# Optimization experiments

Hardware: AMD Instinct MI355X
Metric: run time of the kernel (lower is better)

The kernel has to match this reference:

```python
import jax, jax.numpy as jnp
import numpy as np

N_NODES = 50000
N_EDGES = 400000
H, D = 4, 32  # num_heads, per-head dim
NEG_SLOPE = 0.1


def setup_inputs() -> dict:
    key = jax.random.key(0)
    ks = jax.random.split(key, 12)
    inp = {
        'features': jax.random.normal(ks[0], (N_NODES, 256), jnp.float32) * 0.1,
        'src': jax.random.randint(ks[1], (N_EDGES,), 0, N_NODES, jnp.int32),
        'dst': jax.random.randint(ks[2], (N_EDGES,), 0, N_NODES, jnp.int32),
        'w': jax.random.uniform(ks[3], (N_EDGES,), jnp.float32),
        'W1': jax.random.normal(ks[4], (256, 128), jnp.float32) * 0.05,
        'al1': jax.random.normal(ks[5], (H, D), jnp.float32) * 0.1,
        'ar1': jax.random.normal(ks[6], (H, D), jnp.float32) * 0.1,
        'W2': jax.random.normal(ks[7], (128, 128), jnp.float32) * 0.05,
        'al2': jax.random.normal(ks[8], (H, D), jnp.float32) * 0.1,
        'ar2': jax.random.normal(ks[9], (H, D), jnp.float32) * 0.1,
        'Wout': jax.random.normal(ks[10], (256, 128), jnp.float32) * 0.05,
        'bout': jnp.zeros((128,), jnp.float32),
    }
    return inp


def _gat_layer(x, W, al, ar, src, dst, w):
    # x: [N, in_dim] -> ft: [N, H, D]
    ft = (x @ W).reshape(-1, H, D)
    el = jnp.einsum('nhd,hd->nh', ft, al)  # left attention logits per node
    er = jnp.einsum('nhd,hd->nh', ft, ar)
    # edge logits: leaky_relu(el[src] + er[dst]), then edge-weight scaling
    e = jax.nn.leaky_relu(el[src] + er[dst], negative_slope=NEG_SLOPE)  # [E, H]
    e = w[:, None] * e
    # segment softmax over incoming edges of each destination node
    m = jax.ops.segment_max(e, dst, num_segments=N_NODES)  # [N, H]
    a = jnp.exp(e - m[dst])
    s = jax.ops.segment_sum(a, dst, num_segments=N_NODES)
    a = a / s[dst]  # [E, H]
    # weighted scatter-sum aggregation: rst[dst] += a * ft[src]
    msg = ft[src] * a[:, :, None]  # [E, H, D]
    rst = jax.ops.segment_sum(msg, dst, num_segments=N_NODES)  # [N, H, D]
    # activation=relu, then concat heads (contiguous -> reshape)
    return jax.nn.relu(rst).reshape(-1, H * D)


def reference(features, src, dst, w, W1, al1, ar1, W2, al2, ar2, Wout, bout):
    x1 = _gat_layer(features, W1, al1, ar1, src, dst, w)  # [N, 128]
    x2 = _gat_layer(x1, W2, al2, ar2, src, dst, w)        # [N, 128]
    h = jnp.concatenate([x1, x2], axis=-1)                # [N, 256]
    return h @ Wout + bout                                # [N, 128]
```

## Files before the change

kernel.cpp:

```cpp
#include <hip/hip_runtime.h>
#include <math.h>

#define NHEAD 4
#define HDIM 32
#define NEG_SLOPE 0.1f

typedef unsigned short u16;
typedef unsigned int u32;
typedef _Float16 f16;
typedef f16 f16x2 __attribute__((ext_vector_type(2)));
typedef f16 f16x4 __attribute__((ext_vector_type(4)));
typedef f16 f16x8 __attribute__((ext_vector_type(8)));
typedef float f32x4 __attribute__((ext_vector_type(4)));

#define GLLDS16(g, l) __builtin_amdgcn_global_load_lds( \
    (const __attribute__((address_space(1))) void*)(g), \
    (__attribute__((address_space(3))) void*)(l), 16, 0, 0)


__device__ __forceinline__ void cast_panel(const float* __restrict__ W,
                                           const float* __restrict__ al,
                                           const float* __restrict__ ar,
                                           u16* __restrict__ bp, int t, int NC) {
    int per_kt = NC * 16;
    int kt = t / per_kt;
    int rem = t - kt * per_kt;
    int nt = rem >> 8;
    int w32 = rem & 255;
    int kg = w32 >> 6;
    int col = (w32 >> 2) & 15;
    int kp = (w32 & 3) * 2;
    int n = nt * 16 + col;
    int k = kt * 32 + kg * 8 + kp;
    float v0 = 0.f, v1 = 0.f;
    if (n < 128) {
        v0 = W[(size_t)k * 128 + n];
        v1 = W[(size_t)(k + 1) * 128 + n];
    } else if (n < 136) {
        const float* av = (n < 132) ? al : ar;
        int h = (n < 132) ? (n - 128) : (n - 132);
        float s0 = 0.f, s1 = 0.f;
        for (int d = 0; d < 32; d++) {
            float a = av[h * 32 + d];
            s0 += W[(size_t)k * 128 + h * 32 + d] * a;
            s1 += W[(size_t)(k + 1) * 128 + h * 32 + d] * a;
        }
        v0 = s0; v1 = s1;
    }
    f16x2 p;
    p.x = (f16)v0; p.y = (f16)v1;
    *(f16x2*)&((u32*)bp)[t] = p;
}

__global__ void histcast_k(const int* __restrict__ dst, int* __restrict__ cnt, int E,
                           const float* __restrict__ W1, const float* __restrict__ al1,
                           const float* __restrict__ ar1, u16* __restrict__ b1,
                           const float* __restrict__ W2, const float* __restrict__ al2,
                           const float* __restrict__ ar2, u16* __restrict__ b2,
                           const float* __restrict__ W3, u16* __restrict__ b3) {
    int t = blockIdx.x * 256 + threadIdx.x;
    if (t < E) atomicAdd(&cnt[dst[t]], 1);
    if (t < 18432) cast_panel(W1, al1, ar1, b1, t, 144);
    else if (t < 27648) cast_panel(W2, al2, ar2, b2, t - 18432, 144);
    else if (t < 44032) cast_panel(W3, nullptr, nullptr, b3, t - 27648, 128);
}


__global__ void assign_k(const int* __restrict__ cnt, int* __restrict__ start,
                         int* __restrict__ ctr, int N) {
    __shared__ int s[256];
    __shared__ int base;
    int t = threadIdx.x;
    int i = blockIdx.x * 256 + t;
    int v = (i < N) ? cnt[i] : 0;
    s[t] = v;
    __syncthreads();
    int incl = v;
    for (int off = 1; off < 256; off <<= 1) {
        int add = (t >= off) ? s[t - off] : 0;
        __syncthreads();
        incl += add;
        s[t] = incl;
        __syncthreads();
    }
    if (t == 255) base = atomicAdd(ctr, incl);
    __syncthreads();
    if (i < N) start[i] = base + incl - v;
}

__global__ void scatter_k(const int* __restrict__ src, const int* __restrict__ dst,
                          const float* __restrict__ w, const int* __restrict__ start,
                          int* __restrict__ fill, int2* __restrict__ edge_s, int E) {
    int e = blockIdx.x * 256 + threadIdx.x;
    if (e >= E) return;
    int d = dst[e];
    int p = atomicAdd(&fill[d], 1);
    edge_s[start[d] + p] = make_int2(src[e], __float_as_int(w[e]));
}


template <int NT>
__global__ __launch_bounds__(256) void gemm_h_k(
        const void* __restrict__ Av, int a_is_f16, int lda,
        const u16* __restrict__ Bp,
        const float* __restrict__ bias, float* __restrict__ Cf,
        u16* __restrict__ Ch, float* __restrict__ el, float* __restrict__ er,
        int M, int K) {
    __shared__ u16 As[2048];
    __shared__ u16 Bs[NT * 512];
    int tid = threadIdx.x;
    int w = tid >> 6, lane = tid & 63;
    int row0 = blockIdx.x * 64;
    int mrow = lane & 15;

    f32x4 acc[NT];
#pragma unroll
    for (int nt = 0; nt < NT; nt++) acc[nt] = (f32x4){0.f, 0.f, 0.f, 0.f};

    for (int k0 = 0; k0 < K; k0 += 32) {
        int kt = k0 >> 5;
#pragma unroll
        for (int i = 0; i < (NT * 64 + 255) / 256; i++) {
            int c = tid + i * 256;
            if (c < NT * 64)
                GLLDS16(Bp + (size_t)kt * (NT * 512) + (size_t)c * 8, &Bs[c * 8]);
        }
        if (a_is_f16) {
            const u16* Ah = (const u16*)Av;
            int c = tid;
            int rblk = c >> 6, kg = (c >> 4) & 3, rr = c & 15;
            GLLDS16(Ah + (size_t)(row0 + rblk * 16 + rr) * lda + k0 + kg * 8,
                    &As[c * 8]);
        } else {
            const float* Af = (const float*)Av;
            int c = tid;
            int rblk = c >> 6, kg = (c >> 4) & 3, rr = c & 15;
            int row = min(row0 + rblk * 16 + rr, M - 1);
            const float* ap = &Af[(size_t)row * lda + k0 + kg * 8];
            float4 v0 = *(const float4*)ap;
            float4 v1 = *(const float4*)(ap + 4);
            f16x8 p;
            p[0] = (f16)v0.x; p[1] = (f16)v0.y; p[2] = (f16)v0.z; p[3] = (f16)v0.w;
            p[4] = (f16)v1.x; p[5] = (f16)v1.y; p[6] = (f16)v1.z; p[7] = (f16)v1.w;
            *(f16x8*)&As[c * 8] = p;
        }
        __syncthreads();

        f16x8 ah = *(const f16x8*)&As[w * 512 + lane * 8];
#pragma unroll
        for (int nt = 0; nt < NT; nt++) {
            f16x8 bh = *(const f16x8*)&Bs[nt * 512 + lane * 8];
            acc[nt] = __builtin_amdgcn_mfma_f32_16x16x32_f16(ah, bh, acc[nt], 0, 0, 0);
        }
        __syncthreads();
    }

    int rbase = row0 + w * 16 + (lane >> 4) * 4;
#pragma unroll
    for (int nt = 0; nt < 8; nt++) {
        int col = nt * 16 + mrow;
        float bv = bias ? bias[col] : 0.f;
        f32x4 v = acc[nt];
#pragma unroll
        for (int reg = 0; reg < 4; reg++) {
            int rr = rbase + reg;
            if (rr < M) {
                float val = v[reg] + bv;
                if (Cf) Cf[(size_t)rr * 128 + col] = val;
                if (Ch) *(f16*)&Ch[(size_t)rr * 128 + col] = (f16)val;
            }
        }
    }
    if (NT == 9) {
        f32x4 v = acc[8];
#pragma unroll
        for (int reg = 0; reg < 4; reg++) {
            int rr = rbase + reg;
            if (rr < M) {
                if (mrow < 4) el[rr * 4 + mrow] = v[reg];
                else if (mrow < 8) er[rr * 4 + (mrow - 4)] = v[reg];
            }
        }
    }
}


__device__ __forceinline__ float lrelu(float x) {
    return x > 0.f ? x : NEG_SLOPE * x;
}

__global__ __launch_bounds__(256) void agg_k(const u32* __restrict__ fth2,
                                             const float4* __restrict__ el4,
                                             const float4* __restrict__ er4,
                                             const int2* __restrict__ edge_s,
                                             const int* __restrict__ start,
                                             const int* __restrict__ cnt,
                                             u16* __restrict__ xcat,
                                             int ooff, int N, int ngroups) {
    __shared__ float4 sA[256];
    __shared__ int sS[256];
    int wv = threadIdx.x >> 6;
    int lane = threadIdx.x & 63;
    int head = lane >> 4;
    for (int g = blockIdx.x; g < ngroups; g += gridDim.x) {
        int n = g * 4 + wv;
        if (n >= N) continue;
        int r0 = start[n], deg = cnt[n];
        u16* op = &xcat[(size_t)n * 256 + ooff + 2 * lane];
        if (deg == 0) {
            *(u32*)op = 0;
            continue;
        }
        float4 ern = er4[n];
        float acc0 = 0.f, acc1 = 0.f;
        if (deg <= 64) {
            float4 a = make_float4(0.f, 0.f, 0.f, 0.f);
            int s = 0;
            if (lane < deg) {
                int2 ep = edge_s[r0 + lane];
                s = ep.x;
                float we = __int_as_float(ep.y);
                float4 e = el4[s];
                a.x = __expf(we * lrelu(e.x + ern.x));
                a.y = __expf(we * lrelu(e.y + ern.y));
                a.z = __expf(we * lrelu(e.z + ern.z));
                a.w = __expf(we * lrelu(e.w + ern.w));
            }
            float4 sm = a;
            for (int m = 1; m < deg; m <<= 1) {
                sm.x += __shfl_xor(sm.x, m);
                sm.y += __shfl_xor(sm.y, m);
                sm.z += __shfl_xor(sm.z, m);
                sm.w += __shfl_xor(sm.w, m);
            }
            a.x *= __builtin_amdgcn_rcpf(sm.x);
            a.y *= __builtin_amdgcn_rcpf(sm.y);
            a.z *= __builtin_amdgcn_rcpf(sm.z);
            a.w *= __builtin_amdgcn_rcpf(sm.w);
            sA[wv * 64 + lane] = a;
            sS[wv * 64 + lane] = s;
            const float* sAf = (const float*)&sA[wv * 64];
            const int* sSp = &sS[wv * 64];
            int i = 0;
            for (; i + 8 <= deg; i += 8) {
                float wg[8];
                u32 pp[8];
#pragma unroll
                for (int j = 0; j < 8; j++) {
                    wg[j] = sAf[(i + j) * 4 + head];
                    pp[j] = fth2[(size_t)sSp[i + j] * 64 + lane];
                }
#pragma unroll
                for (int j = 0; j < 8; j++) {
                    f16x2 hp = *(const f16x2*)&pp[j];
                    acc0 += wg[j] * (float)hp.x;
                    acc1 += wg[j] * (float)hp.y;
                }
            }
            for (; i < deg; i++) {
                float wgt = sAf[i * 4 + head];
                u32 p = fth2[(size_t)sSp[i] * 64 + lane];
                f16x2 hp = *(const f16x2*)&p;
                acc0 += wgt * (float)hp.x;
                acc1 += wgt * (float)hp.y;
            }
        } else {
            float4 mx = make_float4(-INFINITY, -INFINITY, -INFINITY, -INFINITY);
            for (int i = lane; i < deg; i += 64) {
                int2 ep = edge_s[r0 + i];
                float we = __int_as_float(ep.y);
                float4 e = el4[ep.x];
                mx.x = fmaxf(mx.x, we * lrelu(e.x + ern.x));
                mx.y = fmaxf(mx.y, we * lrelu(e.y + ern.y));
                mx.z = fmaxf(mx.z, we * lrelu(e.z + ern.z));
                mx.w = fmaxf(mx.w, we * lrelu(e.w + ern.w));
            }
            for (int m = 32; m >= 1; m >>= 1) {
                mx.x = fmaxf(mx.x, __shfl_xor(mx.x, m));
                mx.y = fmaxf(mx.y, __shfl_xor(mx.y, m));
                mx.z = fmaxf(mx.z, __shfl_xor(mx.z, m));
                mx.w = fmaxf(mx.w, __shfl_xor(mx.w, m));
            }
            float4 sm = make_float4(0.f, 0.f, 0.f, 0.f);
            for (int i = lane; i < deg; i += 64) {
                int2 ep = edge_s[r0 + i];
                float we = __int_as_float(ep.y);
                float4 e = el4[ep.x];
                sm.x += __expf(we * lrelu(e.x + ern.x) - mx.x);
                sm.y += __expf(we * lrelu(e.y + ern.y) - mx.y);
                sm.z += __expf(we * lrelu(e.z + ern.z) - mx.z);
                sm.w += __expf(we * lrelu(e.w + ern.w) - mx.w);
            }
            for (int m = 32; m >= 1; m >>= 1) {
                sm.x += __shfl_xor(sm.x, m);
                sm.y += __shfl_xor(sm.y, m);
                sm.z += __shfl_xor(sm.z, m);
                sm.w += __shfl_xor(sm.w, m);
            }
            float4 inv;
            inv.x = 1.f / sm.x; inv.y = 1.f / sm.y;
            inv.z = 1.f / sm.z; inv.w = 1.f / sm.w;
            for (int i = 0; i < deg; i++) {
                int2 ep = edge_s[r0 + i];
                int si = ep.x;
                float we = __int_as_float(ep.y);
                float4 e = el4[si];
                float ax = __expf(we * lrelu(e.x + ern.x) - mx.x) * inv.x;
                float ay = __expf(we * lrelu(e.y + ern.y) - mx.y) * inv.y;
                float az = __expf(we * lrelu(e.z + ern.z) - mx.z) * inv.z;
                float aw = __expf(we * lrelu(e.w + ern.w) - mx.w) * inv.w;
                float wgt = head == 0 ? ax : (head == 1 ? ay : (head == 2 ? az : aw));
                u32 p = fth2[(size_t)si * 64 + lane];
                f16x2 hp = *(const f16x2*)&p;
                acc0 += wgt * (float)hp.x;
                acc1 += wgt * (float)hp.y;
            }
        }
        f16x2 hv;
        hv.x = (f16)fmaxf(acc0, 0.f);
        hv.y = (f16)fmaxf(acc1, 0.f);
        *(f16x2*)op = hv;
    }
}


extern "C" void kernel_launch(void* const* d_in, const int* in_sizes, int n_in,
                              void* d_out, int out_size, void* d_ws, size_t ws_size,
                              hipStream_t stream) {
    const float* features = (const float*)d_in[0];
    const int* src = (const int*)d_in[1];
    const int* dst = (const int*)d_in[2];
    const float* w = (const float*)d_in[3];
    const float* W1 = (const float*)d_in[4];
    const float* al1 = (const float*)d_in[5];
    const float* ar1 = (const float*)d_in[6];
    const float* W2 = (const float*)d_in[7];
    const float* al2 = (const float*)d_in[8];
    const float* ar2 = (const float*)d_in[9];
    const float* Wout = (const float*)d_in[10];
    const float* bout = (const float*)d_in[11];
    float* out = (float*)d_out;

    int N = in_sizes[0] / 256;
    int E = in_sizes[1];
    int Mpad = ((N + 127) / 128) * 128;

    char* ws = (char*)d_ws;
    size_t off = 0;
    auto alloc = [&](size_t bytes) -> void* {
        void* p = ws + off;
        off = (off + bytes + 255) & ~(size_t)255;
        return p;
    };
    size_t Nr = ((size_t)N * 4 + 255) & ~(size_t)255;
    int* cnt = (int*)alloc(2 * Nr + 256);
    int* fill = (int*)((char*)cnt + Nr);
    int* ctr = (int*)((char*)cnt + 2 * Nr);
    int* start = (int*)alloc((size_t)N * 4);
    int2* edge_s = (int2*)alloc((size_t)E * 8);
    u16* fth = (u16*)alloc((size_t)Mpad * 128 * 2);
    float* el = (float*)alloc((size_t)N * 4 * 4);
    float* er = (float*)alloc((size_t)N * 4 * 4);
    u16* xcat = (u16*)alloc((size_t)Mpad * 256 * 2);
    u16* b1 = (u16*)alloc((size_t)18432 * 4);
    u16* b2 = (u16*)alloc((size_t)9216 * 4);
    u16* b3 = (u16*)alloc((size_t)16384 * 4);
    (void)ws_size; (void)n_in; (void)out_size;

    hipMemsetAsync(cnt, 0, 2 * Nr + 256, stream);

    int eb = (E + 255) / 256;
    int nb = (N + 255) / 256;
    int ng = (N + 3) / 4;
    int ab = ng < 2048 ? ng : 2048;
    int gb = Mpad / 64;

    histcast_k<<<eb, 256, 0, stream>>>(dst, cnt, E, W1, al1, ar1, b1,
                                       W2, al2, ar2, b2, Wout, b3);
    assign_k<<<nb, 256, 0, stream>>>(cnt, start, ctr, N);
    scatter_k<<<eb, 256, 0, stream>>>(src, dst, w, start, fill, edge_s, E);

    gemm_h_k<9><<<gb, 256, 0, stream>>>(features, 0, 256, b1, nullptr,
                                        nullptr, fth, el, er, N, 256);
    agg_k<<<ab, 256, 0, stream>>>((const u32*)fth, (const float4*)el, (const float4*)er,
                                  edge_s, start, cnt, xcat, 0, N, ng);

    gemm_h_k<9><<<gb, 256, 0, stream>>>(xcat, 1, 256, b2, nullptr,
                                        nullptr, fth, el, er, N, 128);
    agg_k<<<ab, 256, 0, stream>>>((const u32*)fth, (const float4*)el, (const float4*)er,
                                  edge_s, start, cnt, xcat, 128, N, ng);

    gemm_h_k<8><<<gb, 256, 0, stream>>>(xcat, 1, 256, b3, bout,
                                        out, nullptr, nullptr, nullptr, N, 256);
}
```

Baseline: 258.7 us.

## Fuse all GAT stages into one persistent kernel with grid-wide barriers

Replaces eight separate kernel launches with a single persistent kernel whose blocks loop over work in each phase and meet at a hand-rolled atomic grid barrier. The grid is sized from occupancy, capped at 1024 blocks. Layer-1 GEMM is placed after scatter without a barrier, so it overlaps the edge sort. The goal is to remove launch gaps and tail idle time between small phases. The costs are barrier spin overhead, reduced parallelism in the grid-strided GEMM and agg loops, and reliance on all blocks being co-resident.

```diff
diff --git a/kernel.cpp b/kernel.cpp
--- a/kernel.cpp
+++ b/kernel.cpp
@@ -1,21 +1,46 @@
 #include <hip/hip_runtime.h>
 #include <math.h>
 
-#define NHEAD 4
-#define HDIM 32
 #define NEG_SLOPE 0.1f
 
 typedef unsigned short u16;
 typedef unsigned int u32;
 typedef _Float16 f16;
 typedef f16 f16x2 __attribute__((ext_vector_type(2)));
-typedef f16 f16x4 __attribute__((ext_vector_type(4)));
 typedef f16 f16x8 __attribute__((ext_vector_type(8)));
 typedef float f32x4 __attribute__((ext_vector_type(4)));
 
 #define GLLDS16(g, l) __builtin_amdgcn_global_load_lds( \
     (const __attribute__((address_space(1))) void*)(g), \
     (__attribute__((address_space(3))) void*)(l), 16, 0, 0)
+
+struct P {
+    const float* features; const int* src; const int* dst; const float* w;
+    const float* W1; const float* al1; const float* ar1;
+    const float* W2; const float* al2; const float* ar2;
+    const float* W3; const float* bout; float* out;
+    int* cnt; int* fill; int* ctr; int* bar; int* start; int2* edge_s;
+    u16* fth; float* el; float* er; u16* xcat;
+    u16* b1; u16* b2; u16* b3;
+    int N, E, Mpad;
+};
+
+
+__device__ __forceinline__ void gsync(int* bar, int slot) {
+    __syncthreads();
+    if (threadIdx.x == 0) {
+        __threadfence();
+        int* a = &bar[slot * 16];
+        int prev = __hip_atomic_fetch_add(a, 1, __ATOMIC_ACQ_REL, __HIP_MEMORY_SCOPE_AGENT);
+        if (prev == (int)gridDim.x - 1) {
+            __hip_atomic_store(a + 1, 1, __ATOMIC_RELEASE, __HIP_MEMORY_SCOPE_AGENT);
+        } else {
+            while (!__hip_atomic_load(a + 1, __ATOMIC_ACQUIRE, __HIP_MEMORY_SCOPE_AGENT))
+                __builtin_amdgcn_s_sleep(4);
+        }
+    }
+    __syncthreads();
+}
 
 
 __device__ __forceinline__ void cast_panel(const float* __restrict__ W,
@@ -38,175 +63,177 @@
         v1 = W[(size_t)(k + 1) * 128 + n];
     } else if (n < 136) {
         const float* av = (n < 132) ? al : ar;
-        int h = (n < 132) ? (n - 128) : (n - 132);
-        float s0 = 0.f, s1 = 0.f;
-        for (int d = 0; d < 32; d++) {
-            float a = av[h * 32 + d];
-            s0 += W[(size_t)k * 128 + h * 32 + d] * a;
-            s1 += W[(size_t)(k + 1) * 128 + h * 32 + d] * a;
-        }
-        v0 = s0; v1 = s1;
-    }
-    f16x2 p;
-    p.x = (f16)v0; p.y = (f16)v1;
-    *(f16x2*)&((u32*)bp)[t] = p;
-}
-
-__global__ void histcast_k(const int* __restrict__ dst, int* __restrict__ cnt, int E,
-                           const float* __restrict__ W1, const float* __restrict__ al1,
-                           const float* __restrict__ ar1, u16* __restrict__ b1,
-                           const float* __restrict__ W2, const float* __restrict__ al2,
-                           const float* __restrict__ ar2, u16* __restrict__ b2,
-                           const float* __restrict__ W3, u16* __restrict__ b3) {
-    int t = blockIdx.x * 256 + threadIdx.x;
-    if (t < E) atomicAdd(&cnt[dst[t]], 1);
-    if (t < 18432) cast_panel(W1, al1, ar1, b1, t, 144);
-    else if (t < 27648) cast_panel(W2, al2, ar2, b2, t - 18432, 144);
-    else if (t < 44032) cast_panel(W3, nullptr, nullptr, b3, t - 27648, 128);
-}
-
-
-__global__ void assign_k(const int* __restrict__ cnt, int* __restrict__ start,
-                         int* __restrict__ ctr, int N) {
-    __shared__ int s[256];
-    __shared__ int base;
+        if (av) {
+            int h = (n < 132) ? (n - 128) : (n - 132);
+            float s0 = 0.f, s1 = 0.f;
+            for (int d = 0; d < 32; d++) {
+                float a = av[h * 32 + d];
+                s0 += W[(size_t)k * 128 + h * 32 + d] * a;
+                s1 += W[(size_t)(k + 1) * 128 + h * 32 + d] * a;
+            }
+            v0 = s0; v1 = s1;
+        }
+    }
+    f16x2 pk;
+    pk.x = (f16)v0; pk.y = (f16)v1;
+    *(f16x2*)&((u32*)bp)[t] = pk;
+}
+
+
+__device__ void phase_hist(const P& p) {
+    int gsz = gridDim.x * 256;
+    for (int t = blockIdx.x * 256 + threadIdx.x; t < p.E; t += gsz) {
+        atomicAdd(&p.cnt[p.dst[t]], 1);
+        if (t < 18432) cast_panel(p.W1, p.al1, p.ar1, p.b1, t, 144);
+        else if (t < 27648) cast_panel(p.W2, p.al2, p.ar2, p.b2, t - 18432, 144);
+        else if (t < 46080) cast_panel(p.W3, nullptr, nullptr, p.b3, t - 27648, 144);
+    }
+}
+
+__device__ void phase_assign(const P& p, char* sh) {
+    int* s = (int*)sh;
+    int* basep = s + 256;
     int t = threadIdx.x;
-    int i = blockIdx.x * 256 + t;
-    int v = (i < N) ? cnt[i] : 0;
-    s[t] = v;
-    __syncthreads();
-    int incl = v;
-    for (int off = 1; off < 256; off <<= 1) {
-        int add = (t >= off) ? s[t - off] : 0;
+    int chunks = (p.N + 255) >> 8;
+    for (int c = blockIdx.x; c < chunks; c += gridDim.x) {
+        int i = c * 256 + t;
+        int v = (i < p.N) ? p.cnt[i] : 0;
+        s[t] = v;
         __syncthreads();
-        incl += add;
-        s[t] = incl;
+        int incl = v;
+        for (int off = 1; off < 256; off <<= 1) {
+            int add = (t >= off) ? s[t - off] : 0;
+            __syncthreads();
+            incl += add;
+            s[t] = incl;
+            __syncthreads();
+        }
+        if (t == 255) *basep = atomicAdd(p.ctr, incl);
         __syncthreads();
-    }
-    if (t == 255) base = atomicAdd(ctr, incl);
-    __syncthreads();
-    if (i < N) start[i] = base + incl - v;
-}
-
-__global__ void scatter_k(const int* __restrict__ src, const int* __restrict__ dst,
-                          const float* __restrict__ w, const int* __restrict__ start,
-                          int* __restrict__ fill, int2* __restrict__ edge_s, int E) {
-    int e = blockIdx.x * 256 + threadIdx.x;
-    if (e >= E) return;
-    int d = dst[e];
-    int p = atomicAdd(&fill[d], 1);
-    edge_s[start[d] + p] = make_int2(src[e], __float_as_int(w[e]));
-}
-
-
-template <int NT>
-__global__ __launch_bounds__(256) void gemm_h_k(
-        const void* __restrict__ Av, int a_is_f16, int lda,
-        const u16* __restrict__ Bp,
-        const float* __restrict__ bias, float* __restrict__ Cf,
-        u16* __restrict__ Ch, float* __restrict__ el, float* __restrict__ er,
-        int M, int K) {
-    __shared__ u16 As[2048];
-    __shared__ u16 Bs[NT * 512];
+        if (i < p.N) p.start[i] = *basep + incl - v;
+        __syncthreads();
+    }
+}
+
+__device__ void phase_scatter(const P& p) {
+    int gsz = gridDim.x * 256;
+    for (int e = blockIdx.x * 256 + threadIdx.x; e < p.E; e += gsz) {
+        int d = p.dst[e];
+        int pos = atomicAdd(&p.fill[d], 1);
+        p.edge_s[p.start[d] + pos] = make_int2(p.src[e], __float_as_int(p.w[e]));
+    }
+}
+
+__device__ void gemm_core(const void* Av, int a_is_f16, int lda, const u16* Bp,
+                          const float* bias, float* Cf, u16* Ch,
+                          float* el, float* er, int M, int K, char* shmem) {
+    u16* As = (u16*)shmem;
+    u16* Bs = (u16*)(shmem + 4096);
     int tid = threadIdx.x;
-    int w = tid >> 6, lane = tid & 63;
-    int row0 = blockIdx.x * 64;
+    int wv = tid >> 6, lane = tid & 63;
     int mrow = lane & 15;
-
-    f32x4 acc[NT];
-#pragma unroll
-    for (int nt = 0; nt < NT; nt++) acc[nt] = (f32x4){0.f, 0.f, 0.f, 0.f};
-
-    for (int k0 = 0; k0 < K; k0 += 32) {
-        int kt = k0 >> 5;
-#pragma unroll
-        for (int i = 0; i < (NT * 64 + 255) / 256; i++) {
-            int c = tid + i * 256;
-            if (c < NT * 64)
-                GLLDS16(Bp + (size_t)kt * (NT * 512) + (size_t)c * 8, &Bs[c * 8]);
-        }
-        if (a_is_f16) {
-            const u16* Ah = (const u16*)Av;
+    int tiles = (M + 63) >> 6;
+    for (int t = blockIdx.x; t < tiles; t += gridDim.x) {
+        int row0 = t * 64;
+        f32x4 acc[9];
+#pragma unroll
+        for (int nt = 0; nt < 9; nt++) acc[nt] = (f32x4){0.f, 0.f, 0.f, 0.f};
+        for (int k0 = 0; k0 < K; k0 += 32) {
+            int kt = k0 >> 5;
+#pragma unroll
+            for (int i = 0; i < 3; i++) {
+                int c = tid + i * 256;
+                if (c < 576)
+                    GLLDS16(Bp + (size_t)kt * 4608 + (size_t)c * 8, &Bs[c * 8]);
+            }
             int c = tid;
             int rblk = c >> 6, kg = (c >> 4) & 3, rr = c & 15;
-            GLLDS16(Ah + (size_t)(row0 + rblk * 16 + rr) * lda + k0 + kg * 8,
-                    &As[c * 8]);
-        } else {
-            const float* Af = (const float*)Av;
-            int c = tid;
-            int rblk = c >> 6, kg = (c >> 4) & 3, rr = c & 15;
-            int row = min(row0 + rblk * 16 + rr, M - 1);
-            const float* ap = &Af[(size_t)row * lda + k0 + kg * 8];
-            float4 v0 = *(const float4*)ap;
-            float4 v1 = *(const float4*)(ap + 4);
-            f16x8 p;
-            p[0] = (f16)v0.x; p[1] = (f16)v0.y; p[2] = (f16)v0.z; p[3] = (f16)v0.w;
-            p[4] = (f16)v1.x; p[5] = (f16)v1.y; p[6] = (f16)v1.z; p[7] = (f16)v1.w;
-            *(f16x8*)&As[c * 8] = p;
-        }
-        __syncthreads();
-
-        f16x8 ah = *(const f16x8*)&As[w * 512 + lane * 8];
-#pragma unroll
-        for (int nt = 0; nt < NT; nt++) {
-            f16x8 bh = *(const f16x8*)&Bs[nt * 512 + lane * 8];
-            acc[nt] = __builtin_amdgcn_mfma_f32_16x16x32_f16(ah, bh, acc[nt], 0, 0, 0);
-        }
-        __syncthreads();
-    }
-
-    int rbase = row0 + w * 16 + (lane >> 4) * 4;
-#pragma unroll
-    for (int nt = 0; nt < 8; nt++) {
-        int col = nt * 16 + mrow;
-        float bv = bias ? bias[col] : 0.f;
-        f32x4 v = acc[nt];
-#pragma unroll
-        for (int reg = 0; reg < 4; reg++) {
-            int rr = rbase + reg;
-            if (rr < M) {
-                float val = v[reg] + bv;
-                if (Cf) Cf[(size_t)rr * 128 + col] = val;
-                if (Ch) *(f16*)&Ch[(size_t)rr * 128 + col] = (f16)val;
-            }
-        }
-    }
-    if (NT == 9) {
-        f32x4 v = acc[8];
-#pragma unroll
-        for (int reg = 0; reg < 4; reg++) {
-            int rr = rbase + reg;
-            if (rr < M) {
-                if (mrow < 4) el[rr * 4 + mrow] = v[reg];
-                else if (mrow < 8) er[rr * 4 + (mrow - 4)] = v[reg];
-            }
-        }
-    }
-}
-
+            if (a_is_f16) {
+                const u16* Ah = (const u16*)Av;
+                GLLDS16(Ah + (size_t)(row0 + rblk * 16 + rr) * lda + k0 + kg * 8,
+                        &As[c * 8]);
+            } else {
+                const float* Af = (const float*)Av;
+                int row = row0 + rblk * 16 + rr;
+                if (row > M - 1) row = M - 1;
+                const float* ap = &Af[(size_t)row * lda + k0 + kg * 8];
+                float4 v0 = *(const float4*)ap;
+                float4 v1 = *(const float4*)(ap + 4);
+                f16x8 pk;
+                pk[0] = (f16)v0.x; pk[1] = (f16)v0.y; pk[2] = (f16)v0.z; pk[3] = (f16)v0.w;
+                pk[4] = (f16)v1.x; pk[5] = (f16)v1.y; pk[6] = (f16)v1.z; pk[7] = (f16)v1.w;
+                *(f16x8*)&As[c * 8] = pk;
+            }
+            __syncthreads();
+            f16x8 ah = *(const f16x8*)&As[wv * 512 + lane * 8];
+#pragma unroll
+            for (int nt = 0; nt < 9; nt++) {
+                f16x8 bh = *(const f16x8*)&Bs[nt * 512 + lane * 8];
+                acc[nt] = __builtin_amdgcn_mfma_f32_16x16x32_f16(ah, bh, acc[nt], 0, 0, 0);
+            }
+            __syncthreads();
+        }
+        int rbase = row0 + wv * 16 + (lane >> 4) * 4;
+#pragma unroll
+        for (int nt = 0; nt < 8; nt++) {
+            int col = nt * 16 + mrow;
+            float bv = bias ? bias[col] : 0.f;
+            f32x4 v = acc[nt];
+#pragma unroll
+            for (int reg = 0; reg < 4; reg++) {
+                int r2 = rbase + reg;
+                if (r2 < M) {
+                    float val = v[reg] + bv;
+                    if (Cf) Cf[(size_t)r2 * 128 + col] = val;
+                    if (Ch) *(f16*)&Ch[(size_t)r2 * 128 + col] = (f16)val;
+                }
+            }
+        }
+        if (el) {
+            f32x4 v = acc[8];
+#pragma unroll
+            for (int reg = 0; reg < 4; reg++) {
+                int r2 = rbase + reg;
+                if (r2 < M) {
+                    if (mrow < 4) el[r2 * 4 + mrow] = v[reg];
+                    else if (mrow < 8) er[r2 * 4 + (mrow - 4)] = v[reg];
+                }
+            }
+        }
+    }
+}
+
+__device__ void gemm_sel(const P& p, int which, char* sh) {
+    if (which == 1)
+        gemm_core(p.features, 0, 256, p.b1, nullptr, nullptr, p.fth, p.el, p.er,
+                  p.N, 256, sh);
+    else if (which == 2)
+        gemm_core(p.xcat, 1, 256, p.b2, nullptr, nullptr, p.fth, p.el, p.er,
+                  p.N, 128, sh);
+    else
+        gemm_core(p.xcat, 1, 256, p.b3, p.bout, p.out, nullptr, nullptr, nullptr,
+                  p.N, 256, sh);
+}
 
 __device__ __forceinline__ float lrelu(float x) {
     return x > 0.f ? x : NEG_SLOPE * x;
 }
 
-__global__ __launch_bounds__(256) void agg_k(const u32* __restrict__ fth2,
-                                             const float4* __restrict__ el4,
-                                             const float4* __restrict__ er4,
-                                             const int2* __restrict__ edge_s,
-                                             const int* __restrict__ start,
-                                             const int* __restrict__ cnt,
-                                             u16* __restrict__ xcat,
-                                             int ooff, int N, int ngroups) {
-    __shared__ float4 sA[256];
-    __shared__ int sS[256];
+__device__ void phase_agg(const P& p, int ooff, char* sh) {
+    float4* sA = (float4*)sh;
+    int* sS = (int*)(sh + 4096);
+    const u32* fth2 = (const u32*)p.fth;
+    const float4* el4 = (const float4*)p.el;
+    const float4* er4 = (const float4*)p.er;
     int wv = threadIdx.x >> 6;
     int lane = threadIdx.x & 63;
     int head = lane >> 4;
+    int ngroups = (p.N + 3) >> 2;
     for (int g = blockIdx.x; g < ngroups; g += gridDim.x) {
         int n = g * 4 + wv;
-        if (n >= N) continue;
-        int r0 = start[n], deg = cnt[n];
-        u16* op = &xcat[(size_t)n * 256 + ooff + 2 * lane];
+        if (n >= p.N) continue;
+        int r0 = p.start[n], deg = p.cnt[n];
+        u16* op = &p.xcat[(size_t)n * 256 + ooff + 2 * lane];
         if (deg == 0) {
             *(u32*)op = 0;
             continue;
@@ -217,7 +244,7 @@
             float4 a = make_float4(0.f, 0.f, 0.f, 0.f);
             int s = 0;
             if (lane < deg) {
-                int2 ep = edge_s[r0 + lane];
+                int2 ep = p.edge_s[r0 + lane];
                 s = ep.x;
                 float we = __int_as_float(ep.y);
                 float4 e = el4[s];
@@ -259,15 +286,15 @@
             }
             for (; i < deg; i++) {
                 float wgt = sAf[i * 4 + head];
-                u32 p = fth2[(size_t)sSp[i] * 64 + lane];
-                f16x2 hp = *(const f16x2*)&p;
+                u32 pv = fth2[(size_t)sSp[i] * 64 + lane];
+                f16x2 hp = *(const f16x2*)&pv;
                 acc0 += wgt * (float)hp.x;
                 acc1 += wgt * (float)hp.y;
             }
         } else {
             float4 mx = make_float4(-INFINITY, -INFINITY, -INFINITY, -INFINITY);
             for (int i = lane; i < deg; i += 64) {
-                int2 ep = edge_s[r0 + i];
+                int2 ep = p.edge_s[r0 + i];
                 float we = __int_as_float(ep.y);
                 float4 e = el4[ep.x];
                 mx.x = fmaxf(mx.x, we * lrelu(e.x + ern.x));
@@ -283,7 +310,7 @@
             }
             float4 sm = make_float4(0.f, 0.f, 0.f, 0.f);
             for (int i = lane; i < deg; i += 64) {
-                int2 ep = edge_s[r0 + i];
+                int2 ep = p.edge_s[r0 + i];
                 float we = __int_as_float(ep.y);
                 float4 e = el4[ep.x];
                 sm.x += __expf(we * lrelu(e.x + ern.x) - mx.x);
@@ -301,7 +328,7 @@
             inv.x = 1.f / sm.x; inv.y = 1.f / sm.y;
             inv.z = 1.f / sm.z; inv.w = 1.f / sm.w;
             for (int i = 0; i < deg; i++) {
-                int2 ep = edge_s[r0 + i];
+                int2 ep = p.edge_s[r0 + i];
                 int si = ep.x;
                 float we = __int_as_float(ep.y);
                 float4 e = el4[si];
@@ -310,8 +337,8 @@
                 float az = __expf(we * lrelu(e.z + ern.z) - mx.z) * inv.z;
                 float aw = __expf(we * lrelu(e.w + ern.w) - mx.w) * inv.w;
                 float wgt = head == 0 ? ax : (head == 1 ? ay : (head == 2 ? az : aw));
-                u32 p = fth2[(size_t)si * 64 + lane];
-                f16x2 hp = *(const f16x2*)&p;
+                u32 pv = fth2[(size_t)si * 64 + lane];
+                f16x2 hp = *(const f16x2*)&pv;
                 acc0 += wgt * (float)hp.x;
                 acc1 += wgt * (float)hp.y;
             }
@@ -324,72 +351,108 @@
 }
 
 
+__global__ __launch_bounds__(256, 4) void k_fused(P p) {
+    alignas(16) __shared__ char sh[13312];
+    phase_hist(p);
+    gsync(p.bar, 0);
+    phase_assign(p, sh);
+    gsync(p.bar, 1);
+    phase_scatter(p);
+    gemm_sel(p, 1, sh);
+    gsync(p.bar, 2);
+    phase_agg(p, 0, sh);
+    gsync(p.bar, 3);
+    gemm_sel(p, 2, sh);
+    gsync(p.bar, 4);
+    phase_agg(p, 128, sh);
+    gsync(p.bar, 5);
+    gemm_sel(p, 3, sh);
+}
+
+
+__global__ __launch_bounds__(256) void k_p1(P p) { phase_hist(p); }
+__global__ __launch_bounds__(256) void k_assign(P p) {
+    alignas(16) __shared__ char sh[2048];
+    phase_assign(p, sh);
+}
+__global__ __launch_bounds__(256) void k_scatter(P p) { phase_scatter(p); }
+__global__ __launch_bounds__(256) void k_gemm(P p, int which) {
+    alignas(16) __shared__ char sh[13312];
+    gemm_sel(p, which, sh);
+}
+__global__ __launch_bounds__(256) void k_agg(P p, int ooff) {
+    alignas(16) __shared__ char sh[8192];
+    phase_agg(p, ooff, sh);
+}
+
+
 extern "C" void kernel_launch(void* const* d_in, const int* in_sizes, int n_in,
                               void* d_out, int out_size, void* d_ws, size_t ws_size,
                               hipStream_t stream) {
-    const float* features = (const float*)d_in[0];
-    const int* src = (const int*)d_in[1];
-    const int* dst = (const int*)d_in[2];
-    const float* w = (const float*)d_in[3];
-    const float* W1 = (const float*)d_in[4];
-    const float* al1 = (const float*)d_in[5];
-    const float* ar1 = (const float*)d_in[6];
-    const float* W2 = (const float*)d_in[7];
-    const float* al2 = (const float*)d_in[8];
-    const float* ar2 = (const float*)d_in[9];
-    const float* Wout = (const float*)d_in[10];
-    const float* bout = (const float*)d_in[11];
-    float* out = (float*)d_out;
-
-    int N = in_sizes[0] / 256;
-    int E = in_sizes[1];
-    int Mpad = ((N + 127) / 128) * 128;
+    P p;
+    p.features = (const float*)d_in[0];
+    p.src = (const int*)d_in[1];
+    p.dst = (const int*)d_in[2];
+    p.w = (const float*)d_in[3];
+    p.W1 = (const float*)d_in[4];
+    p.al1 = (const float*)d_in[5];
+    p.ar1 = (const float*)d_in[6];
+    p.W2 = (const float*)d_in[7];
+    p.al2 = (const float*)d_in[8];
+    p.ar2 = (const float*)d_in[9];
+    p.W3 = (const float*)d_in[10];
+    p.bout = (const float*)d_in[11];
+    p.out = (float*)d_out;
+
+    p.N = in_sizes[0] / 256;
+    p.E = in_sizes[1];
+    p.Mpad = ((p.N + 127) / 128) * 128;
 
     char* ws = (char*)d_ws;
     size_t off = 0;
     auto alloc = [&](size_t bytes) -> void* {
-        void* p = ws + off;
+        void* q = ws + off;
         off = (off + bytes + 255) & ~(size_t)255;
-        return p;
+        return q;
     };
-    size_t Nr = ((size_t)N * 4 + 255) & ~(size_t)255;
-    int* cnt = (int*)alloc(2 * Nr + 256);
-    int* fill = (int*)((char*)cnt + Nr);
-    int* ctr = (int*)((char*)cnt + 2 * Nr);
-    int* start = (int*)alloc((size_t)N * 4);
-    int2* edge_s = (int2*)alloc((size_t)E * 8);
-    u16* fth = (u16*)alloc((size_t)Mpad * 128 * 2);
-    float* el = (float*)alloc((size_t)N * 4 * 4);
-    float* er = (float*)alloc((size_t)N * 4 * 4);
-    u16* xcat = (u16*)alloc((size_t)Mpad * 256 * 2);
-    u16* b1 = (u16*)alloc((size_t)18432 * 4);
-    u16* b2 = (u16*)alloc((size_t)9216 * 4);
-    u16* b3 = (u16*)alloc((size_t)16384 * 4);
+    size_t Nr = ((size_t)p.N * 4 + 255) & ~(size_t)255;
+    p.cnt = (int*)alloc(2 * Nr + 1024);
+    p.fill = (int*)((char*)p.cnt + Nr);
+    p.ctr = (int*)((char*)p.cnt + 2 * Nr);
+    p.bar = p.ctr + 64;
+    p.start = (int*)alloc((size_t)p.N * 4);
+    p.edge_s = (int2*)alloc((size_t)p.E * 8);
+    p.fth = (u16*)alloc((size_t)p.Mpad * 128 * 2);
+    p.el = (float*)alloc((size_t)p.N * 4 * 4);
+    p.er = (float*)alloc((size_t)p.N * 4 * 4);
+    p.xcat = (u16*)alloc((size_t)p.Mpad * 256 * 2);
+    p.b1 = (u16*)alloc((size_t)18432 * 4);
+    p.b2 = (u16*)alloc((size_t)9216 * 4);
+    p.b3 = (u16*)alloc((size_t)18432 * 4);
     (void)ws_size; (void)n_in; (void)out_size;
 
-    hipMemsetAsync(cnt, 0, 2 * Nr + 256, stream);
-
-    int eb = (E + 255) / 256;
-    int nb = (N + 255) / 256;
-    int ng = (N + 3) / 4;
-    int ab = ng < 2048 ? ng : 2048;
-    int gb = Mpad / 64;
-
-    histcast_k<<<eb, 256, 0, stream>>>(dst, cnt, E, W1, al1, ar1, b1,
-                                       W2, al2, ar2, b2, Wout, b3);
-    assign_k<<<nb, 256, 0, stream>>>(cnt, start, ctr, N);
-    scatter_k<<<eb, 256, 0, stream>>>(src, dst, w, start, fill, edge_s, E);
-
-    gemm_h_k<9><<<gb, 256, 0, stream>>>(features, 0, 256, b1, nullptr,
-                                        nullptr, fth, el, er, N, 256);
-    agg_k<<<ab, 256, 0, stream>>>((const u32*)fth, (const float4*)el, (const float4*)er,
-                                  edge_s, start, cnt, xcat, 0, N, ng);
-
-    gemm_h_k<9><<<gb, 256, 0, stream>>>(xcat, 1, 256, b2, nullptr,
-                                        nullptr, fth, el, er, N, 128);
-    agg_k<<<ab, 256, 0, stream>>>((const u32*)fth, (const float4*)el, (const float4*)er,
-                                  edge_s, start, cnt, xcat, 128, N, ng);
-
-    gemm_h_k<8><<<gb, 256, 0, stream>>>(xcat, 1, 256, b3, bout,
-                                        out, nullptr, nullptr, nullptr, N, 256);
-}
+    hipMemsetAsync(p.cnt, 0, 2 * Nr + 1024, stream);
+
+    static int s_grid = -2;
+    if (s_grid == -2) {
+        int b = 0;
+        hipError_t e = hipOccupancyMaxActiveBlocksPerMultiprocessor(&b, k_fused, 256, 0);
+        s_grid = (e == hipSuccess && b >= 1) ? (b * 256 < 1024 ? b * 256 : 1024) : 0;
+    }
+
+    if (s_grid > 0) {
+        k_fused<<<s_grid, 256, 0, stream>>>(p);
+    } else {
+        int eb = (p.E + 255) / 256;
+        int cb = (p.N + 255) / 256;
+        int gb = p.Mpad / 64;
+        k_p1<<<eb, 256, 0, stream>>>(p);
+        k_assign<<<cb, 256, 0, stream>>>(p);
+        k_scatter<<<eb, 256, 0, stream>>>(p);
+        k_gemm<<<gb, 256, 0, stream>>>(p, 1);
+        k_agg<<<2048, 256, 0, stream>>>(p, 0);
+        k_gemm<<<gb, 256, 0, stream>>>(p, 2);
+        k_agg<<<2048, 256, 0, stream>>>(p, 128);
+        k_gemm<<<gb, 256, 0, stream>>>(p, 3);
+    }
+}
```

Measured after the change: 795.8 us. 208% more time.

## Merge edge scatter into first GEMM launch and double GEMM K-step

Applied to the files above, without the earlier changes.

The edge-scatter kernel becomes extra blocks of the first projection GEMM launch, so CSR construction and the layer-1 GEMM run side by side in one launch instead of back to back. The GEMM body moves into a shared device function that now stages 64 K-columns per iteration (two 32-wide slices), which halves the barrier count and gives more MFMA work per sync. In exchange each block uses more shared memory, which may lower occupancy, and the grid of the merged launch now holds two unrelated block types.

```diff
diff --git a/kernel.cpp b/kernel.cpp
--- a/kernel.cpp
+++ b/kernel.cpp
@@ -1,15 +1,12 @@
 #include <hip/hip_runtime.h>
 #include <math.h>
 
-#define NHEAD 4
-#define HDIM 32
 #define NEG_SLOPE 0.1f
 
 typedef unsigned short u16;
 typedef unsigned int u32;
 typedef _Float16 f16;
 typedef f16 f16x2 __attribute__((ext_vector_type(2)));
-typedef f16 f16x4 __attribute__((ext_vector_type(4)));
 typedef f16 f16x8 __attribute__((ext_vector_type(8)));
 typedef float f32x4 __attribute__((ext_vector_type(4)));
 
@@ -88,74 +85,69 @@
     if (i < N) start[i] = base + incl - v;
 }
 
-__global__ void scatter_k(const int* __restrict__ src, const int* __restrict__ dst,
-                          const float* __restrict__ w, const int* __restrict__ start,
-                          int* __restrict__ fill, int2* __restrict__ edge_s, int E) {
-    int e = blockIdx.x * 256 + threadIdx.x;
-    if (e >= E) return;
-    int d = dst[e];
-    int p = atomicAdd(&fill[d], 1);
-    edge_s[start[d] + p] = make_int2(src[e], __float_as_int(w[e]));
-}
-
 
 template <int NT>
-__global__ __launch_bounds__(256) void gemm_h_k(
+__device__ __forceinline__ void gemm_tile(
         const void* __restrict__ Av, int a_is_f16, int lda,
         const u16* __restrict__ Bp,
         const float* __restrict__ bias, float* __restrict__ Cf,
         u16* __restrict__ Ch, float* __restrict__ el, float* __restrict__ er,
-        int M, int K) {
-    __shared__ u16 As[2048];
-    __shared__ u16 Bs[NT * 512];
+        int M, int K, int tile, char* shmem) {
+    u16* As = (u16*)shmem;
+    u16* Bs = (u16*)(shmem + 8192);
     int tid = threadIdx.x;
-    int w = tid >> 6, lane = tid & 63;
-    int row0 = blockIdx.x * 64;
+    int wv = tid >> 6, lane = tid & 63;
     int mrow = lane & 15;
+    int row0 = tile * 64;
 
     f32x4 acc[NT];
 #pragma unroll
     for (int nt = 0; nt < NT; nt++) acc[nt] = (f32x4){0.f, 0.f, 0.f, 0.f};
 
-    for (int k0 = 0; k0 < K; k0 += 32) {
-        int kt = k0 >> 5;
-#pragma unroll
-        for (int i = 0; i < (NT * 64 + 255) / 256; i++) {
+    for (int k0 = 0; k0 < K; k0 += 64) {
+        int kt0 = k0 >> 5;
+        const u16* Bsrc = Bp + (size_t)kt0 * (NT * 512);
+#pragma unroll
+        for (int i = 0; i < (2 * NT * 64 + 255) / 256; i++) {
             int c = tid + i * 256;
-            if (c < NT * 64)
-                GLLDS16(Bp + (size_t)kt * (NT * 512) + (size_t)c * 8, &Bs[c * 8]);
-        }
-        if (a_is_f16) {
-            const u16* Ah = (const u16*)Av;
-            int c = tid;
-            int rblk = c >> 6, kg = (c >> 4) & 3, rr = c & 15;
-            GLLDS16(Ah + (size_t)(row0 + rblk * 16 + rr) * lda + k0 + kg * 8,
-                    &As[c * 8]);
-        } else {
-            const float* Af = (const float*)Av;
-            int c = tid;
-            int rblk = c >> 6, kg = (c >> 4) & 3, rr = c & 15;
-            int row = min(row0 + rblk * 16 + rr, M - 1);
-            const float* ap = &Af[(size_t)row * lda + k0 + kg * 8];
-            float4 v0 = *(const float4*)ap;
-            float4 v1 = *(const float4*)(ap + 4);
-            f16x8 p;
-            p[0] = (f16)v0.x; p[1] = (f16)v0.y; p[2] = (f16)v0.z; p[3] = (f16)v0.w;
-            p[4] = (f16)v1.x; p[5] = (f16)v1.y; p[6] = (f16)v1.z; p[7] = (f16)v1.w;
-            *(f16x8*)&As[c * 8] = p;
+            if (c < 2 * NT * 64) GLLDS16(Bsrc + (size_t)c * 8, &Bs[c * 8]);
+        }
+#pragma unroll
+        for (int i = 0; i < 2; i++) {
+            int c = tid + i * 256;
+            int slice = c >> 8, w32 = c & 255;
+            int rblk = w32 >> 6, kg = (w32 >> 4) & 3, rr = w32 & 15;
+            int row = row0 + rblk * 16 + rr;
+            int k = k0 + slice * 32 + kg * 8;
+            if (a_is_f16) {
+                const u16* Ah = (const u16*)Av;
+                GLLDS16(Ah + (size_t)row * lda + k, &As[c * 8]);
+            } else {
+                const float* Af = (const float*)Av;
+                if (row > M - 1) row = M - 1;
+                const float* ap = &Af[(size_t)row * lda + k];
+                float4 v0 = *(const float4*)ap;
+                float4 v1 = *(const float4*)(ap + 4);
+                f16x8 pk;
+                pk[0] = (f16)v0.x; pk[1] = (f16)v0.y; pk[2] = (f16)v0.z; pk[3] = (f16)v0.w;
+                pk[4] = (f16)v1.x; pk[5] = (f16)v1.y; pk[6] = (f16)v1.z; pk[7] = (f16)v1.w;
+                *(f16x8*)&As[c * 8] = pk;
+            }
         }
         __syncthreads();
-
-        f16x8 ah = *(const f16x8*)&As[w * 512 + lane * 8];
-#pragma unroll
-        for (int nt = 0; nt < NT; nt++) {
-            f16x8 bh = *(const f16x8*)&Bs[nt * 512 + lane * 8];
-            acc[nt] = __builtin_amdgcn_mfma_f32_16x16x32_f16(ah, bh, acc[nt], 0, 0, 0);
+#pragma unroll
+        for (int kk = 0; kk < 2; kk++) {
+            f16x8 ah = *(const f16x8*)&As[kk * 2048 + wv * 512 + lane * 8];
+#pragma unroll
+            for (int nt = 0; nt < NT; nt++) {
+                f16x8 bh = *(const f16x8*)&Bs[kk * (NT * 512) + nt * 512 + lane * 8];
+                acc[nt] = __builtin_amdgcn_mfma_f32_16x16x32_f16(ah, bh, acc[nt], 0, 0, 0);
+            }
         }
         __syncthreads();
     }
 
-    int rbase = row0 + w * 16 + (lane >> 4) * 4;
+    int rbase = row0 + wv * 16 + (lane >> 4) * 4;
 #pragma unroll
     for (int nt = 0; nt < 8; nt++) {
         int col = nt * 16 + mrow;
@@ -180,6 +172,37 @@
                 if (mrow < 4) el[rr * 4 + mrow] = v[reg];
                 else if (mrow < 8) er[rr * 4 + (mrow - 4)] = v[reg];
             }
+        }
+    }
+}
+
+template <int NT>
+__global__ __launch_bounds__(256) void gemm_k(
+        const void* __restrict__ Av, int a_is_f16, int lda,
+        const u16* __restrict__ Bp, const float* __restrict__ bias,
+        float* __restrict__ Cf, u16* __restrict__ Ch,
+        float* __restrict__ el, float* __restrict__ er, int M, int K) {
+    alignas(16) __shared__ char sh[8192 + NT * 2048];
+    gemm_tile<NT>(Av, a_is_f16, lda, Bp, bias, Cf, Ch, el, er, M, K, blockIdx.x, sh);
+}
+
+__global__ __launch_bounds__(256) void g1s_k(
+        const float* __restrict__ features, const u16* __restrict__ b1,
+        u16* __restrict__ fth, float* __restrict__ el, float* __restrict__ er,
+        int M, int gb,
+        const int* __restrict__ src, const int* __restrict__ dst,
+        const float* __restrict__ w, const int* __restrict__ start,
+        int* __restrict__ fill, int2* __restrict__ edge_s, int E) {
+    alignas(16) __shared__ char sh[8192 + 9 * 2048];
+    if ((int)blockIdx.x < gb) {
+        gemm_tile<9>(features, 0, 256, b1, nullptr, nullptr, fth, el, er,
+                     M, 256, blockIdx.x, sh);
+    } else {
+        int e = (blockIdx.x - gb) * 256 + threadIdx.x;
+        if (e < E) {
+            int d = dst[e];
+            int pos = atomicAdd(&fill[d], 1);
+            edge_s[start[d] + pos] = make_int2(src[e], __float_as_int(w[e]));
         }
     }
 }
@@ -367,7 +390,7 @@
     u16* b3 = (u16*)alloc((size_t)16384 * 4);
     (void)ws_size; (void)n_in; (void)out_size;
 
-    hipMemsetAsync(cnt, 0, 2 * Nr + 256, stream);
+    (void)hipMemsetAsync(cnt, 0, 2 * Nr + 256, stream);
 
     int eb = (E + 255) / 256;
     int nb = (N + 255) / 256;
@@ -378,18 +401,17 @@
     histcast_k<<<eb, 256, 0, stream>>>(dst, cnt, E, W1, al1, ar1, b1,
                                        W2, al2, ar2, b2, Wout, b3);
     assign_k<<<nb, 256, 0, stream>>>(cnt, start, ctr, N);
-    scatter_k<<<eb, 256, 0, stream>>>(src, dst, w, start, fill, edge_s, E);
-
-    gemm_h_k<9><<<gb, 256, 0, stream>>>(features, 0, 256, b1, nullptr,
-                                        nullptr, fth, el, er, N, 256);
+
+    g1s_k<<<gb + eb, 256, 0, stream>>>(features, b1, fth, el, er, N, gb,
+                                       src, dst, w, start, fill, edge_s, E);
     agg_k<<<ab, 256, 0, stream>>>((const u32*)fth, (const float4*)el, (const float4*)er,
                                   edge_s, start, cnt, xcat, 0, N, ng);
 
-    gemm_h_k<9><<<gb, 256, 0, stream>>>(xcat, 1, 256, b2, nullptr,
-                                        nullptr, fth, el, er, N, 128);
+    gemm_k<9><<<gb, 256, 0, stream>>>(xcat, 1, 256, b2, nullptr,
+                                      nullptr, fth, el, er, N, 128);
     agg_k<<<ab, 256, 0, stream>>>((const u32*)fth, (const float4*)el, (const float4*)er,
                                   edge_s, start, cnt, xcat, 128, N, ng);
 
-    gemm_h_k<8><<<gb, 256, 0, stream>>>(xcat, 1, 256, b3, bout,
-                                        out, nullptr, nullptr, nullptr, N, 256);
-}
+    gemm_k<8><<<gb, 256, 0, stream>>>(xcat, 1, 256, b3, bout,
+                                      out, nullptr, nullptr, nullptr, N, 256);
+}
```

After: 247.6 us. 1.04x faster.
